# Kernel tuning notes

Measured on AMD Instinct MI355X. Metric: run time of the kernel, lower is better.

The kernel has to match this reference:

```python
import jax, jax.numpy as jnp
import numpy as np

# --- static config (matches init_kwargs) ---
N = 10000          # nodes
E = 160000         # edges
MULT = 16          # multiplicity (in and out)
NL = 2             # number of irreps (lvals = [0, 1])
DIM = 4            # 1 + 3 spherical dims
EDGE_DIM = 32
HID = 128
RANK = 8           # low-rank radial weight rank
H = 4              # attention heads
HM = MULT // H     # head multiplicity
IDX = np.array([0, 1, 1, 1])  # irrep index for each of the DIM positions


def _radial(ef, w1, bb1, wl, bl, wr, br):
    """Low-rank radial weight: (E, edge_dim) -> (E, NL*MULT, NL*MULT)."""
    h = jax.nn.gelu(ef @ w1 + bb1, approximate=False)
    left = (h @ wl + bl).reshape(-1, NL * MULT, RANK)
    right = (h @ wr + br).reshape(-1, RANK, NL * MULT)
    return left @ right


def _conv(b1, b2, ef, f, src, w1, bb1, wl, bl, wr, br):
    """Equivariant convolution: gather -> basis contract -> radial bmm -> basis."""
    rw = _radial(ef, w1, bb1, wl, bl, wr, br)          # (E, 2*MULT, 2*MULT)
    f_src = f[src]                                      # (E, MULT, DIM)
    t = jnp.einsum('emd,edl->eml', f_src, b1)           # (E, MULT, NL)
    t = t.reshape(E, MULT * NL)                         # row-major, matches torch view
    t = jnp.einsum('erc,ec->er', rw, t)                 # (E, NL*MULT)
    t = t.reshape(E, MULT, NL)                          # (E, out_mult, nl2)
    return jnp.einsum('eml,eld->emd', t, b2)            # (E, MULT, DIM)


def reference(b1, b2, edge_feats, f, src_idx, dst_idx,
              q_w, q_b,
              k_w1, k_b1, k_wl, k_bl, k_wr, k_br,
              v_w1, v_b1, v_wl, v_bl, v_wr, v_br):
    # --- Q: equivariant linear on node features (per-irrep weights) ---
    W = q_w.reshape(NL, MULT, MULT)[IDX]                # (DIM, out_mult, in_mult)
    q = jnp.einsum('dom,nmd->nod', W, f)                # (N, MULT, DIM)
    q = q.at[:, :, 0].add(q_b[:, 0])                    # bias on scalar (l=0) slot

    # --- K, V: equivariant convolutions over edges ---
    k = _conv(b1, b2, edge_feats, f, src_idx, k_w1, k_b1, k_wl, k_bl, k_wr, k_br)
    v = _conv(b1, b2, edge_feats, f, src_idx, v_w1, v_b1, v_wl, v_bl, v_wr, v_br)

    # --- multi-head node_wise attention scores ---
    qh = q.reshape(N, H, HM * DIM)
    kh = k.reshape(E, H, HM * DIM)
    scale = jnp.sqrt(jnp.asarray(HM * DIM, q.dtype))
    scores = jnp.sum(qh[dst_idx] * kh, axis=-1) / scale  # (E, H)

    # --- segment softmax over edges grouped by destination node ---
    m = jax.ops.segment_max(scores, dst_idx, num_segments=N)       # (N, H)
    ex = jnp.exp(scores - m[dst_idx])
    den = jax.ops.segment_sum(ex, dst_idx, num_segments=N)         # (N, H)
    alpha = ex / jnp.maximum(den[dst_idx], 1e-9)                   # (E, H)

    # --- weighted scatter-reduce of values ---
    vh = v.reshape(E, H, HM * DIM)
    out = jax.ops.segment_sum(alpha[..., None] * vh, dst_idx, num_segments=N)
    return out.reshape(N, MULT, DIM)


def setup_inputs() -> dict:
    key = jax.random.key(0)
    ks = jax.random.split(key, 24)
    s = 0.05
    inp = {
        'b1': jax.random.normal(ks[0], (E, DIM, NL), jnp.float32),
        'b2': jax.random.normal(ks[1], (E, NL, DIM), jnp.float32),
        'edge_feats': jax.random.normal(ks[2], (E, EDGE_DIM), jnp.float32),
        'f': jax.random.normal(ks[3], (N, MULT, DIM), jnp.float32),
        'src_idx': jax.random.randint(ks[4], (E,), 0, N),
        'dst_idx': jax.random.randint(ks[5], (E,), 0, N),
        # Q equivariant linear
        'q_w': jax.random.normal(ks[6], (NL * MULT, MULT), jnp.float32) * s,
        'q_b': jnp.zeros((MULT, 1), jnp.float32),
    }
    for i, p in enumerate(['k', 'v']):
        base = 8 + i * 6
        inp[p + '_w1'] = jax.random.normal(ks[base + 0], (EDGE_DIM, HID), jnp.float32) * s
        inp[p + '_b1'] = jnp.zeros((HID,), jnp.float32)
        inp[p + '_wl'] = jax.random.normal(ks[base + 2], (HID, NL * MULT * RANK), jnp.float32) * s
        inp[p + '_bl'] = jnp.zeros((NL * MULT * RANK,), jnp.float32)
        inp[p + '_wr'] = jax.random.normal(ks[base + 4], (HID, RANK * NL * MULT), jnp.float32) * s
        inp[p + '_br'] = jnp.zeros((RANK * NL * MULT,), jnp.float32)
    return inp
```

## Files before the change

### kernel.cpp

```cpp
#include <hip/hip_runtime.h>
#include <hip/hip_bf16.h>
#include <math.h>

#define NNODES 10000
#define NEDGE  160000

typedef unsigned short u16;
using bf16x8 = __attribute__((ext_vector_type(8))) short;
using u16x8  = __attribute__((ext_vector_type(8))) unsigned short;
using f32x4  = __attribute__((ext_vector_type(4))) float;

static __device__ __forceinline__ u16 f2bf(float x) {
  unsigned u = __float_as_uint(x);
  u += 0x7FFFu + ((u >> 16) & 1u);
  return (u16)(u >> 16);
}
static __device__ __forceinline__ float bf2f(u16 h) {
  return __uint_as_float(((unsigned)h) << 16);
}
static __device__ __forceinline__ unsigned pack_bf16(float a, float b) {
  __hip_bfloat162 h = __float22bfloat162_rn(make_float2(a, b));
  return *(unsigned*)&h;
}
static __device__ __forceinline__ float fast_gelu(float x) {
  float y = x * __builtin_fmaf(0.07135481283f, x * x, 1.5957691216f);
  float e = __expf(y);
  return x - x * __builtin_amdgcn_rcpf(e + 1.0f);
}
static __device__ __forceinline__ float dpp_red16(float p) {
  p += __int_as_float(__builtin_amdgcn_update_dpp(0, __float_as_int(p), 0xB1,  0xF, 0xF, true));
  p += __int_as_float(__builtin_amdgcn_update_dpp(0, __float_as_int(p), 0x4E,  0xF, 0xF, true));
  p += __int_as_float(__builtin_amdgcn_update_dpp(0, __float_as_int(p), 0x141, 0xF, 0xF, true));
  p += __int_as_float(__builtin_amdgcn_update_dpp(0, __float_as_int(p), 0x140, 0xF, 0xF, true));
  return p;
}

__global__ void zero_cnt_kernel(int* __restrict__ cnt) {
  int i = blockIdx.x * 256 + threadIdx.x;
  if (i < NNODES) cnt[i] = 0;
}

__global__ void __launch_bounds__(256) setup_kernel(
    const float* __restrict__ kwr, const float* __restrict__ kwl,
    const float* __restrict__ vwr, const float* __restrict__ vwl,
    u16* __restrict__ Wsw,
    const float* __restrict__ kw1, const float* __restrict__ vw1,
    u16* __restrict__ W1sw,
    const float* __restrict__ f, const float* __restrict__ qw,
    const float* __restrict__ qb, float* __restrict__ q,
    const int* __restrict__ dst, int* __restrict__ cnt) {
  int b = blockIdx.x, tid = threadIdx.x;
  if (b < 512) {
    int idx = b * 256 + tid;
    int slot = idx >> 15;
    int w = idx & 32767;
    int j = w & 7, lane = (w >> 3) & 63, ks = (w >> 9) & 3, tg = w >> 11;
    int k   = ks * 32 + ((lane >> 4) << 3) + j;
    int col = (tg << 4) + (lane & 15);
    const float* s = (slot == 0) ? kwr : (slot == 1) ? kwl : (slot == 2) ? vwr : vwl;
    Wsw[idx] = f2bf(s[k * 256 + col]);
  } else if (b < 544) {
    int idx = (b - 512) * 256 + tid;
    int slot = idx >> 12;
    int w = idx & 4095;
    int j = w & 7, lane = (w >> 3) & 63, nt = w >> 9;
    int k   = ((lane >> 4) << 3) + j;
    int col = (nt << 4) + (lane & 15);
    const float* s = (slot == 0) ? kw1 : vw1;
    W1sw[idx] = f2bf(s[k * 128 + col]);
  } else if (b < 1169) {
    int i = (b - 544) * 256 + tid;
    if (i >= NNODES * 16) return;
    int n = i >> 4, o = i & 15;
    const float* frow = f + (size_t)n * 64;
    float o0 = 0.f, o1 = 0.f, o2 = 0.f, o3 = 0.f;
#pragma unroll
    for (int m = 0; m < 16; ++m) {
      float w0 = qw[o * 16 + m];
      float w1 = qw[(16 + o) * 16 + m];
      o0 += w0 * frow[m * 4 + 0];
      o1 += w1 * frow[m * 4 + 1];
      o2 += w1 * frow[m * 4 + 2];
      o3 += w1 * frow[m * 4 + 3];
    }
    o0 += qb[o];
    float4 r = make_float4(o0, o1, o2, o3);
    *(float4*)(q + (size_t)i * 4) = r;
  } else {
    int e = (b - 1169) * 256 + tid;
    atomicAdd(&cnt[dst[e]], 1);
  }
}

__global__ void __launch_bounds__(1024) csr_scan_kernel(
    const int* __restrict__ cnt, int* __restrict__ rowptr, int* __restrict__ cursor) {
  __shared__ int part[1024];
  int t = threadIdx.x;
  int base = t * 10;
  int s = 0;
#pragma unroll
  for (int i = 0; i < 10; ++i) { int idx = base + i; if (idx < NNODES) s += cnt[idx]; }
  part[t] = s;
  __syncthreads();
  for (int o = 1; o < 1024; o <<= 1) {
    int v = (t >= o) ? part[t - o] : 0;
    __syncthreads();
    part[t] += v;
    __syncthreads();
  }
  int run = (t == 0) ? 0 : part[t - 1];
#pragma unroll
  for (int i = 0; i < 10; ++i) {
    int idx = base + i;
    if (idx < NNODES) { rowptr[idx] = run; cursor[idx] = run; run += cnt[idx]; }
  }
  if (t == 1023) rowptr[NNODES] = run;
}

__global__ void __launch_bounds__(256) fill_t_kernel(
    const int* __restrict__ dst, const int* __restrict__ src,
    const float* __restrict__ f, const float* __restrict__ b1,
    const float* __restrict__ b2, const float* __restrict__ ef,
    int* __restrict__ cursor, char* __restrict__ comb) {
  int e = blockIdx.x * 256 + threadIdx.x;
  int pos = atomicAdd(&cursor[dst[e]], 1);
  char* rb = comb + (size_t)pos * 192;
  const float* frow = f + (size_t)src[e] * 64;
  const float* be = b1 + (size_t)e * 8;
  float b[8];
#pragma unroll
  for (int k = 0; k < 8; ++k) b[k] = be[k];
  uint4* tp = (uint4*)rb;
#pragma unroll
  for (int mh = 0; mh < 4; ++mh) {
    unsigned pk[4];
#pragma unroll
    for (int mi = 0; mi < 4; ++mi) {
      int m = mh * 4 + mi;
      float f0 = frow[m * 4 + 0], f1 = frow[m * 4 + 1], f2 = frow[m * 4 + 2], f3 = frow[m * 4 + 3];
      float t0 = f0 * b[0] + f1 * b[2] + f2 * b[4] + f3 * b[6];
      float t1 = f0 * b[1] + f1 * b[3] + f2 * b[5] + f3 * b[7];
      pk[mi] = pack_bf16(t0, t1);
    }
    tp[mh] = make_uint4(pk[0], pk[1], pk[2], pk[3]);
  }
  const float* efe = ef + (size_t)e * 32;
#pragma unroll
  for (int g = 0; g < 4; ++g) {
    float4 v0 = *(const float4*)&efe[g * 8];
    float4 v1 = *(const float4*)&efe[g * 8 + 4];
    tp[4 + g] = make_uint4(pack_bf16(v0.x, v0.y), pack_bf16(v0.z, v0.w),
                           pack_bf16(v1.x, v1.y), pack_bf16(v1.z, v1.w));
  }
  const float* b2e = b2 + (size_t)e * 8;
  *(float4*)(rb + 128) = *(const float4*)&b2e[0];
  *(float4*)(rb + 144) = *(const float4*)&b2e[4];
}

__global__ void __launch_bounds__(512) conv_fused_kernel(
    const char* __restrict__ comb, const u16* __restrict__ w1sw,
    const float* __restrict__ b1h,
    const u16* __restrict__ wsw_r, const float* __restrict__ br,
    const u16* __restrict__ wsw_l, const float* __restrict__ bl,
    u16* __restrict__ kv) {
  __shared__ alignas(16) u16 sA[64 * 136];
  __shared__ alignas(16) u16 t_s[64 * 40];
  __shared__ alignas(16) float b2_s[64 * 12];
  __shared__ alignas(16) float u_s[64 * 12];
  __shared__ alignas(16) float t2_pool[64 * 36];
  float* t2_s = t2_pool;
  u16*   efs  = (u16*)t2_pool;

  int tid = threadIdx.x;
  int wave = tid >> 6, lane = tid & 63, quad = lane >> 4, l16 = lane & 15;
  size_t i0 = (size_t)blockIdx.x * 64;

  if (tid < 256) {
    int row = tid >> 2, seg = tid & 3;
    *(uint4*)&efs[row * 40 + seg * 8] =
        *(const uint4*)(comb + (i0 + row) * 192 + 64 + seg * 16);
    if (tid < 128) {
      int r2 = tid >> 1, half = tid & 1;
      *(float4*)&b2_s[r2 * 12 + half * 4] =
          *(const float4*)(comb + (i0 + r2) * 192 + 128 + half * 16);
    }
  } else {
    int j = tid - 256;
    int row = j >> 2, seg = j & 3;
    *(uint4*)&t_s[row * 40 + seg * 8] =
        *(const uint4*)(comb + (i0 + row) * 192 + seg * 16);
  }
  __syncthreads();

  {
    bf16x8 aw = *(const bf16x8*)&w1sw[(size_t)(wave * 64 + lane) * 8];
    float4 bias_h = *(const float4*)&b1h[wave * 16 + quad * 4];
#pragma unroll
    for (int nt = 0; nt < 4; ++nt) {
      bf16x8 be = *(const bf16x8*)&efs[(nt * 16 + l16) * 40 + quad * 8];
      f32x4 acch = __builtin_amdgcn_mfma_f32_16x16x32_bf16(aw, be, (f32x4){0.f, 0.f, 0.f, 0.f}, 0, 0, 0);
      unsigned p0 = pack_bf16(fast_gelu(acch[0] + bias_h.x), fast_gelu(acch[1] + bias_h.y));
      unsigned p1 = pack_bf16(fast_gelu(acch[2] + bias_h.z), fast_gelu(acch[3] + bias_h.w));
      *(uint2*)&sA[(nt * 16 + l16) * 136 + wave * 16 + quad * 4] = make_uint2(p0, p1);
    }
  }
  __syncthreads();

  f32x4 accr[2][4], accl[2][4];
#pragma unroll
  for (int mtl = 0; mtl < 2; ++mtl)
#pragma unroll
    for (int nt = 0; nt < 4; ++nt) {
      accr[mtl][nt] = (f32x4){0.f, 0.f, 0.f, 0.f};
      accl[mtl][nt] = (f32x4){0.f, 0.f, 0.f, 0.f};
    }
#pragma unroll
  for (int ks = 0; ks < 4; ++ks) {
    bf16x8 bfrag[4];
#pragma unroll
    for (int nt = 0; nt < 4; ++nt)
      bfrag[nt] = *(const bf16x8*)&sA[(nt * 16 + l16) * 136 + ks * 32 + quad * 8];
#pragma unroll
    for (int mtl = 0; mtl < 2; ++mtl) {
      int mtg = wave * 2 + mtl;
      bf16x8 ar = *(const bf16x8*)&wsw_r[(size_t)((mtg * 4 + ks) * 64 + lane) * 8];
      bf16x8 al = *(const bf16x8*)&wsw_l[(size_t)((mtg * 4 + ks) * 64 + lane) * 8];
#pragma unroll
      for (int nt = 0; nt < 4; ++nt) {
        accr[mtl][nt] = __builtin_amdgcn_mfma_f32_16x16x32_bf16(ar, bfrag[nt], accr[mtl][nt], 0, 0, 0);
        accl[mtl][nt] = __builtin_amdgcn_mfma_f32_16x16x32_bf16(al, bfrag[nt], accl[mtl][nt], 0, 0, 0);
      }
    }
  }

  float4 brv[2], blv[2];
#pragma unroll
  for (int mtl = 0; mtl < 2; ++mtl) {
    int colb = (wave * 2 + mtl) * 16 + quad * 4;
    brv[mtl] = *(const float4*)&br[colb];
    blv[mtl] = *(const float4*)&bl[colb];
  }

#pragma unroll
  for (int nt = 0; nt < 4; ++nt) {
    int e = nt * 16 + l16;
    ushort4 ta = *(const ushort4*)&t_s[e * 40 + 4 * quad];
    ushort4 tb = *(const ushort4*)&t_s[e * 40 + 16 + 4 * quad];
    float s = (accr[0][nt][0] + brv[0].x) * bf2f(ta.x)
            + (accr[0][nt][1] + brv[0].y) * bf2f(ta.y)
            + (accr[0][nt][2] + brv[0].z) * bf2f(ta.z)
            + (accr[0][nt][3] + brv[0].w) * bf2f(ta.w)
            + (accr[1][nt][0] + brv[1].x) * bf2f(tb.x)
            + (accr[1][nt][1] + brv[1].y) * bf2f(tb.y)
            + (accr[1][nt][2] + brv[1].z) * bf2f(tb.z)
            + (accr[1][nt][3] + brv[1].w) * bf2f(tb.w);
    s += __shfl_xor(s, 16);
    s += __shfl_xor(s, 32);
    if (quad == 0) u_s[e * 12 + wave] = s;
  }
  __syncthreads();

#pragma unroll
  for (int nt = 0; nt < 4; ++nt) {
    int e = nt * 16 + l16;
    float4 uv = *(const float4*)&u_s[e * 12 + 4 * (quad & 1)];
#pragma unroll
    for (int mtl = 0; mtl < 2; ++mtl) {
      float s = (accl[mtl][nt][0] + blv[mtl].x) * uv.x
              + (accl[mtl][nt][1] + blv[mtl].y) * uv.y
              + (accl[mtl][nt][2] + blv[mtl].z) * uv.z
              + (accl[mtl][nt][3] + blv[mtl].w) * uv.w;
      s += __shfl_xor(s, 16);
      if ((quad & 1) == 0)
        t2_s[e * 36 + 4 * wave + 2 * mtl + (quad >> 1)] = s;
    }
  }
  __syncthreads();

  {
    int e = tid >> 3, j = tid & 7;
    float4 t2 = *(const float4*)&t2_s[e * 36 + 4 * j];
    float4 b2a = *(const float4*)&b2_s[e * 12 + 0];
    float4 b2b = *(const float4*)&b2_s[e * 12 + 4];
    unsigned q0 = pack_bf16(t2.x * b2a.x + t2.y * b2b.x, t2.x * b2a.y + t2.y * b2b.y);
    unsigned q1 = pack_bf16(t2.x * b2a.z + t2.y * b2b.z, t2.x * b2a.w + t2.y * b2b.w);
    unsigned q2 = pack_bf16(t2.z * b2a.x + t2.w * b2b.x, t2.z * b2a.y + t2.w * b2b.y);
    unsigned q3 = pack_bf16(t2.z * b2a.z + t2.w * b2b.z, t2.z * b2a.w + t2.w * b2b.w);
    *(uint4*)&kv[(i0 + e) * 64 + j * 8] = make_uint4(q0, q1, q2, q3);
  }
}

__global__ void __launch_bounds__(256) attn_gather_kernel(
    const float* __restrict__ q, const u16* __restrict__ kvk,
    const u16* __restrict__ kvv, const int* __restrict__ rowptr,
    float* __restrict__ outp) {
  int tid = threadIdx.x;
  int node = blockIdx.x * 4 + (tid >> 6);
  int lane = tid & 63;
  float qv = q[(size_t)node * 64 + lane];
  int beg = rowptr[node], end = rowptr[node + 1];
  float num = 0.f, den = 0.f;
  int idx = beg;
  for (; idx + 2 <= end; idx += 2) {
    float kf0 = bf2f(kvk[(size_t)idx * 64 + lane]);
    float kf1 = bf2f(kvk[(size_t)(idx + 1) * 64 + lane]);
    float v0  = bf2f(kvv[(size_t)idx * 64 + lane]);
    float v1  = bf2f(kvv[(size_t)(idx + 1) * 64 + lane]);
    float p0 = dpp_red16(qv * kf0);
    float p1 = dpp_red16(qv * kf1);
    float e0 = __expf(p0 * 0.25f);
    float e1 = __expf(p1 * 0.25f);
    den += e0 + e1;
    num += e0 * v0 + e1 * v1;
  }
  if (idx < end) {
    float kf = bf2f(kvk[(size_t)idx * 64 + lane]);
    float p = dpp_red16(qv * kf);
    float exv = __expf(p * 0.25f);
    den += exv;
    num += exv * bf2f(kvv[(size_t)idx * 64 + lane]);
  }
  outp[(size_t)node * 64 + lane] = num / fmaxf(den, 1e-9f);
}

extern "C" void kernel_launch(void* const* d_in, const int* in_sizes, int n_in,
                              void* d_out, int out_size, void* d_ws, size_t ws_size,
                              hipStream_t stream) {
  const float* b1  = (const float*)d_in[0];
  const float* b2  = (const float*)d_in[1];
  const float* ef  = (const float*)d_in[2];
  const float* f   = (const float*)d_in[3];
  const int*   src = (const int*)d_in[4];
  const int*   dst = (const int*)d_in[5];
  const float* qw  = (const float*)d_in[6];
  const float* qb  = (const float*)d_in[7];
  const float* kw1 = (const float*)d_in[8];
  const float* kb1 = (const float*)d_in[9];
  const float* kwl = (const float*)d_in[10];
  const float* kbl = (const float*)d_in[11];
  const float* kwr = (const float*)d_in[12];
  const float* kbr = (const float*)d_in[13];
  const float* vw1 = (const float*)d_in[14];
  const float* vb1 = (const float*)d_in[15];
  const float* vwl = (const float*)d_in[16];
  const float* vbl = (const float*)d_in[17];
  const float* vwr = (const float*)d_in[18];
  const float* vbr = (const float*)d_in[19];
  float* outp = (float*)d_out;

  char* ws = (char*)d_ws;
  size_t off = 0;
  auto alloc = [&](size_t bytes) {
    char* p = ws + off;
    off += (bytes + 511) & ~(size_t)511;
    return p;
  };
  u16*   Wsw  = (u16*)  alloc((size_t)4 * 32768 * 2);
  u16*   W1sw = (u16*)  alloc((size_t)2 * 4096 * 2);
  char*  comb = (char*) alloc((size_t)NEDGE * 192);
  u16*   kvk  = (u16*)  alloc((size_t)NEDGE * 64 * 2);
  u16*   kvv  = (u16*)  alloc((size_t)NEDGE * 64 * 2);
  float* qbuf = (float*)alloc((size_t)NNODES * 64 * 4);
  int*   cnt    = (int*)alloc((size_t)NNODES * 4);
  int*   rowptr = (int*)alloc((size_t)(NNODES + 1) * 4);
  int*   cursor = (int*)alloc((size_t)NNODES * 4);

  zero_cnt_kernel<<<40, 256, 0, stream>>>(cnt);
  setup_kernel<<<1794, 256, 0, stream>>>(kwr, kwl, vwr, vwl, Wsw,
                                         kw1, vw1, W1sw,
                                         f, qw, qb, qbuf, dst, cnt);
  csr_scan_kernel<<<1, 1024, 0, stream>>>(cnt, rowptr, cursor);
  fill_t_kernel<<<625, 256, 0, stream>>>(dst, src, f, b1, b2, ef,
                                         cursor, comb);

  conv_fused_kernel<<<2500, 512, 0, stream>>>(comb, W1sw + 0 * 4096, kb1,
                                              Wsw + 0 * 32768, kbr,
                                              Wsw + 1 * 32768, kbl,
                                              kvk);
  conv_fused_kernel<<<2500, 512, 0, stream>>>(comb, W1sw + 1 * 4096, vb1,
                                              Wsw + 2 * 32768, vbr,
                                              Wsw + 3 * 32768, vbl,
                                              kvv);

  attn_gather_kernel<<<2500, 256, 0, stream>>>(qbuf, kvk, kvv, rowptr, outp);
}
```

Baseline: 249.7 us.

## Fuse attention score and exp into K conv epilogue, drop K buffer

```diff
diff --git a/kernel.cpp b/kernel.cpp
--- a/kernel.cpp
+++ b/kernel.cpp
@@ -26,13 +26,6 @@
   float y = x * __builtin_fmaf(0.07135481283f, x * x, 1.5957691216f);
   float e = __expf(y);
   return x - x * __builtin_amdgcn_rcpf(e + 1.0f);
-}
-static __device__ __forceinline__ float dpp_red16(float p) {
-  p += __int_as_float(__builtin_amdgcn_update_dpp(0, __float_as_int(p), 0xB1,  0xF, 0xF, true));
-  p += __int_as_float(__builtin_amdgcn_update_dpp(0, __float_as_int(p), 0x4E,  0xF, 0xF, true));
-  p += __int_as_float(__builtin_amdgcn_update_dpp(0, __float_as_int(p), 0x141, 0xF, 0xF, true));
-  p += __int_as_float(__builtin_amdgcn_update_dpp(0, __float_as_int(p), 0x140, 0xF, 0xF, true));
-  return p;
 }
 
 __global__ void zero_cnt_kernel(int* __restrict__ cnt) {
@@ -123,7 +116,8 @@
     const float* __restrict__ b2, const float* __restrict__ ef,
     int* __restrict__ cursor, char* __restrict__ comb) {
   int e = blockIdx.x * 256 + threadIdx.x;
-  int pos = atomicAdd(&cursor[dst[e]], 1);
+  int n = dst[e];
+  int pos = atomicAdd(&cursor[n], 1);
   char* rb = comb + (size_t)pos * 192;
   const float* frow = f + (size_t)src[e] * 64;
   const float* be = b1 + (size_t)e * 8;
@@ -155,6 +149,7 @@
   const float* b2e = b2 + (size_t)e * 8;
   *(float4*)(rb + 128) = *(const float4*)&b2e[0];
   *(float4*)(rb + 144) = *(const float4*)&b2e[4];
+  *(int*)(rb + 160) = n;
 }
 
 __global__ void __launch_bounds__(512) conv_fused_kernel(
@@ -162,6 +157,7 @@
     const float* __restrict__ b1h,
     const u16* __restrict__ wsw_r, const float* __restrict__ br,
     const u16* __restrict__ wsw_l, const float* __restrict__ bl,
+    const float* __restrict__ qbuf, float* __restrict__ exs,
     u16* __restrict__ kv) {
   __shared__ alignas(16) u16 sA[64 * 136];
   __shared__ alignas(16) u16 t_s[64 * 40];
@@ -282,43 +278,55 @@
     float4 t2 = *(const float4*)&t2_s[e * 36 + 4 * j];
     float4 b2a = *(const float4*)&b2_s[e * 12 + 0];
     float4 b2b = *(const float4*)&b2_s[e * 12 + 4];
-    unsigned q0 = pack_bf16(t2.x * b2a.x + t2.y * b2b.x, t2.x * b2a.y + t2.y * b2b.y);
-    unsigned q1 = pack_bf16(t2.x * b2a.z + t2.y * b2b.z, t2.x * b2a.w + t2.y * b2b.w);
-    unsigned q2 = pack_bf16(t2.z * b2a.x + t2.w * b2b.x, t2.z * b2a.y + t2.w * b2b.y);
-    unsigned q3 = pack_bf16(t2.z * b2a.z + t2.w * b2b.z, t2.z * b2a.w + t2.w * b2b.w);
-    *(uint4*)&kv[(i0 + e) * 64 + j * 8] = make_uint4(q0, q1, q2, q3);
+    float v0 = t2.x * b2a.x + t2.y * b2b.x;
+    float v1 = t2.x * b2a.y + t2.y * b2b.y;
+    float v2 = t2.x * b2a.z + t2.y * b2b.z;
+    float v3 = t2.x * b2a.w + t2.y * b2b.w;
+    float v4 = t2.z * b2a.x + t2.w * b2b.x;
+    float v5 = t2.z * b2a.y + t2.w * b2b.y;
+    float v6 = t2.z * b2a.z + t2.w * b2b.z;
+    float v7 = t2.z * b2a.w + t2.w * b2b.w;
+    if (exs) {
+      int n = *(const int*)(comb + (i0 + e) * 192 + 160);
+      const float* qr = qbuf + (size_t)n * 64 + j * 8;
+      float4 qa = *(const float4*)&qr[0];
+      float4 qc = *(const float4*)&qr[4];
+      float s = v0 * qa.x + v1 * qa.y + v2 * qa.z + v3 * qa.w
+              + v4 * qc.x + v5 * qc.y + v6 * qc.z + v7 * qc.w;
+      s += __shfl_xor(s, 1);
+      if ((j & 1) == 0)
+        exs[(i0 + e) * 4 + (j >> 1)] = __expf(s * 0.25f);
+    } else {
+      unsigned q0 = pack_bf16(v0, v1);
+      unsigned q1 = pack_bf16(v2, v3);
+      unsigned q2 = pack_bf16(v4, v5);
+      unsigned q3 = pack_bf16(v6, v7);
+      *(uint4*)&kv[(i0 + e) * 64 + j * 8] = make_uint4(q0, q1, q2, q3);
+    }
   }
 }
 
 __global__ void __launch_bounds__(256) attn_gather_kernel(
-    const float* __restrict__ q, const u16* __restrict__ kvk,
-    const u16* __restrict__ kvv, const int* __restrict__ rowptr,
-    float* __restrict__ outp) {
+    const float* __restrict__ exs, const u16* __restrict__ kvv,
+    const int* __restrict__ rowptr, float* __restrict__ outp) {
   int tid = threadIdx.x;
   int node = blockIdx.x * 4 + (tid >> 6);
-  int lane = tid & 63;
-  float qv = q[(size_t)node * 64 + lane];
+  int lane = tid & 63, h = lane >> 4;
   int beg = rowptr[node], end = rowptr[node + 1];
   float num = 0.f, den = 0.f;
   int idx = beg;
   for (; idx + 2 <= end; idx += 2) {
-    float kf0 = bf2f(kvk[(size_t)idx * 64 + lane]);
-    float kf1 = bf2f(kvk[(size_t)(idx + 1) * 64 + lane]);
-    float v0  = bf2f(kvv[(size_t)idx * 64 + lane]);
-    float v1  = bf2f(kvv[(size_t)(idx + 1) * 64 + lane]);
-    float p0 = dpp_red16(qv * kf0);
-    float p1 = dpp_red16(qv * kf1);
-    float e0 = __expf(p0 * 0.25f);
-    float e1 = __expf(p1 * 0.25f);
+    float e0 = exs[(size_t)idx * 4 + h];
+    float e1 = exs[(size_t)(idx + 1) * 4 + h];
+    float v0 = bf2f(kvv[(size_t)idx * 64 + lane]);
+    float v1 = bf2f(kvv[(size_t)(idx + 1) * 64 + lane]);
+    num += e0 * v0 + e1 * v1;
     den += e0 + e1;
-    num += e0 * v0 + e1 * v1;
   }
   if (idx < end) {
-    float kf = bf2f(kvk[(size_t)idx * 64 + lane]);
-    float p = dpp_red16(qv * kf);
-    float exv = __expf(p * 0.25f);
-    den += exv;
-    num += exv * bf2f(kvv[(size_t)idx * 64 + lane]);
+    float e0 = exs[(size_t)idx * 4 + h];
+    num += e0 * bf2f(kvv[(size_t)idx * 64 + lane]);
+    den += e0;
   }
   outp[(size_t)node * 64 + lane] = num / fmaxf(den, 1e-9f);
 }
@@ -358,8 +366,8 @@
   u16*   Wsw  = (u16*)  alloc((size_t)4 * 32768 * 2);
   u16*   W1sw = (u16*)  alloc((size_t)2 * 4096 * 2);
   char*  comb = (char*) alloc((size_t)NEDGE * 192);
-  u16*   kvk  = (u16*)  alloc((size_t)NEDGE * 64 * 2);
   u16*   kvv  = (u16*)  alloc((size_t)NEDGE * 64 * 2);
+  float* exb  = (float*)alloc((size_t)NEDGE * 4 * 4);
   float* qbuf = (float*)alloc((size_t)NNODES * 64 * 4);
   int*   cnt    = (int*)alloc((size_t)NNODES * 4);
   int*   rowptr = (int*)alloc((size_t)(NNODES + 1) * 4);
@@ -376,11 +384,11 @@
   conv_fused_kernel<<<2500, 512, 0, stream>>>(comb, W1sw + 0 * 4096, kb1,
                                               Wsw + 0 * 32768, kbr,
                                               Wsw + 1 * 32768, kbl,
-                                              kvk);
+                                              qbuf, exb, nullptr);
   conv_fused_kernel<<<2500, 512, 0, stream>>>(comb, W1sw + 1 * 4096, vb1,
                                               Wsw + 2 * 32768, vbr,
                                               Wsw + 3 * 32768, vbl,
-                                              kvv);
-
-  attn_gather_kernel<<<2500, 256, 0, stream>>>(qbuf, kvk, kvv, rowptr, outp);
-}
+                                              qbuf, nullptr, kvv);
+
+  attn_gather_kernel<<<2500, 256, 0, stream>>>(exb, kvv, rowptr, outp);
+}
```

New measurement: 246.2 us. Within noise of the previous version (-1.4%).
